# Optimization experiments

Hardware: AMD Instinct MI355X
Metric: run time of the kernel (lower is better)

The kernel has to match this reference:

```python
import jax, jax.numpy as jnp
import numpy as np

N, M, D = 65536, 1024, 2


def setup_inputs() -> dict:
    key = jax.random.key(0)
    k1, k2, k3 = jax.random.split(key, 3)
    sample = jax.random.uniform(k1, (N, D), dtype=jnp.float32)
    mu = jax.random.uniform(k2, (M, D), dtype=jnp.float32)
    # original init: A = 10 * I; add small noise so covariances are anisotropic
    A = 10.0 * jnp.broadcast_to(jnp.eye(D, dtype=jnp.float32), (M, D, D)) \
        + 0.1 * jax.random.normal(k3, (M, D, D), dtype=jnp.float32)
    w = jnp.ones((M, 1), dtype=jnp.float32)
    return {"sample": sample, "mu": mu, "A": A, "w": w}


def reference(sample, mu, A, w):
    # gamma_j = A_j @ A_j^T  -> precision matrices, (M, D, D)
    gamma = jnp.einsum('mde,mfe->mdf', A, A)
    # 2x2 determinant (only case implemented in the original module)
    det = gamma[:, 0, 0] * gamma[:, 1, 1] - gamma[:, 0, 1] * gamma[:, 1, 0]
    # log weights: log_softmax(w) + 0.5 * log det(gamma)
    log_w = jax.nn.log_softmax(w[:, 0], axis=0) + 0.5 * jnp.log(det)  # (M,)
    # Mahalanobis quadratic form q_ij = (x_i - mu_j)^T gamma_j (x_i - mu_j),
    # expanded to avoid materializing an (N, M, D) difference tensor.
    xGx = jnp.einsum('nd,mde,ne->nm', sample, gamma, sample)          # (N, M)
    gm = jnp.einsum('mde,me->md', gamma, mu)                          # (M, D)
    cross = sample @ gm.T                                             # (N, M)
    mGm = jnp.einsum('md,md->m', gm, mu)                              # (M,)
    q = xGx - 2.0 * cross + mGm[None, :]
    # log-likelihood per sample: logsumexp_j (log_w_j - q_ij)
    return jax.nn.logsumexp(log_w[None, :] - q, axis=1)               # (N,)
```

## Files before the change

### kernel.cpp

```cpp
#include <hip/hip_runtime.h>
#include <math.h>

#define LOG2E 1.4426950408889634f
#define LN2   0.6931471805599453f

static constexpr int M = 1024;
static constexpr int N = 65536;


__global__ __launch_bounds__(1024)
void gm_prep(const float* __restrict__ mu,
             const float* __restrict__ A,
             const float* __restrict__ w,
             float* __restrict__ ws) {
    __shared__ float red[1024];
    const int j = threadIdx.x;

    const float4 a = ((const float4*)A)[j];
    const float g00 = a.x*a.x + a.y*a.y;
    const float g01 = a.x*a.z + a.y*a.w;
    const float g11 = a.z*a.z + a.w*a.w;
    const float2 m  = ((const float2*)mu)[j];
    const float gm0 = g00*m.x + g01*m.y;
    const float gm1 = g01*m.x + g11*m.y;
    const float mGm = gm0*m.x + gm1*m.y;
    const float det = g00*g11 - g01*g01;
    const float wj  = w[j];

    red[j] = wj; __syncthreads();
    for (int off = 512; off > 0; off >>= 1) {
        if (j < off) red[j] = fmaxf(red[j], red[j+off]);
        __syncthreads();
    }
    const float wmax = red[0]; __syncthreads();
    red[j] = expf(wj - wmax); __syncthreads();
    for (int off = 512; off > 0; off >>= 1) {
        if (j < off) red[j] = red[j] + red[j+off];
        __syncthreads();
    }
    const float lse = wmax + logf(red[0]); __syncthreads();

    const float log_w = wj - lse + 0.5f * logf(det);

    red[j] = log_w; __syncthreads();
    for (int off = 512; off > 0; off >>= 1) {
        if (j < off) red[j] = fmaxf(red[j], red[j+off]);
        __syncthreads();
    }
    const float L = red[0];

    float* c = ws + j*8;
    c[0] = LOG2E * (log_w - mGm - L);
    c[1] = LOG2E * 2.0f * gm0;
    c[2] = LOG2E * 2.0f * gm1;
    c[3] = -LOG2E * g00;
    c[4] = -LOG2E * 2.0f * g01;
    c[5] = -LOG2E * g11;
    c[6] = 0.0f;
    c[7] = 0.0f;
    if (j == 0) ws[M*8] = LOG2E * L;
}

__global__ __launch_bounds__(256)
void gm_main(const float* __restrict__ sample,
             const float* __restrict__ ws,
             float* __restrict__ out) {
    __shared__ __align__(16) float coef[M*8];
    __shared__ float partial[256];
    __shared__ float sL2;
    const int t = threadIdx.x;

    const float4* wsv = (const float4*)ws;
    float4* cv = (float4*)coef;
    #pragma unroll
    for (int k = 0; k < 8; k++)
        cv[t + 256*k] = wsv[t + 256*k];
    if (t == 0) sL2 = ws[M*8];
    __syncthreads();

    const int lane  = t & 63;
    const int chunk = t >> 6;
    const int i = blockIdx.x*64 + lane;

    const float2 xy = ((const float2*)sample)[i];
    const float x0 = xy.x, x1 = xy.y;
    const float xx = x0*x0, xyp = x0*x1, yy = x1*x1;

    float s0 = 0.0f, s1 = 0.0f;
    const float* c = coef + chunk*256*8;
    #pragma unroll 8
    for (int jj = 0; jj < 256; jj++) {
        const float* cc = c + jj*8;
        const float v = fmaf(cc[5], yy,
                        fmaf(cc[4], xyp,
                        fmaf(cc[3], xx,
                        fmaf(cc[2], x1,
                        fmaf(cc[1], x0, cc[0])))));
        const float e = __builtin_amdgcn_exp2f(v);
        if (jj & 1) s1 += e; else s0 += e;
    }
    partial[t] = s0 + s1;
    __syncthreads();

    if (t < 64) {
        const float s = partial[t] + partial[t+64] + partial[t+128] + partial[t+192];
        out[blockIdx.x*64 + t] = LN2 * (sL2 + __builtin_amdgcn_logf(s));
    }
}

__global__ __launch_bounds__(256)
void gm_fused(const float* __restrict__ sample,
              const float* __restrict__ mu,
              const float* __restrict__ A,
              const float* __restrict__ w,
              float* __restrict__ out) {
    __shared__ __align__(16) float coef[M*8];
    __shared__ float red[256];
    const int t = threadIdx.x;

    float wv[4], c0t[4], c1t[4], c2t[4], c3t[4], c4t[4], c5t[4], dets[4];
    float wmaxl = -3.4e38f;
    #pragma unroll
    for (int k = 0; k < 4; k++) {
        wv[k] = w[t + 256*k];
        wmaxl = fmaxf(wmaxl, wv[k]);
    }
    red[t] = wmaxl; __syncthreads();
    for (int off = 128; off > 0; off >>= 1) {
        if (t < off) red[t] = fmaxf(red[t], red[t+off]);
        __syncthreads();
    }
    const float wmax = red[0]; __syncthreads();
    float se = 0.0f;
    #pragma unroll
    for (int k = 0; k < 4; k++) se += expf(wv[k] - wmax);
    red[t] = se; __syncthreads();
    for (int off = 128; off > 0; off >>= 1) {
        if (t < off) red[t] = red[t] + red[t+off];
        __syncthreads();
    }
    const float lse = wmax + logf(red[0]); __syncthreads();

    float Lml = -3.4e38f;
    float lwk[4];
    #pragma unroll
    for (int k = 0; k < 4; k++) {
        const int j = t + 256*k;
        const float4 a = ((const float4*)A)[j];
        const float g00 = a.x*a.x + a.y*a.y;
        const float g01 = a.x*a.z + a.y*a.w;
        const float g11 = a.z*a.z + a.w*a.w;
        const float2 m  = ((const float2*)mu)[j];
        const float gm0 = g00*m.x + g01*m.y;
        const float gm1 = g01*m.x + g11*m.y;
        const float mGm = gm0*m.x + gm1*m.y;
        dets[k] = g00*g11 - g01*g01;
        lwk[k]  = wv[k] - lse + 0.5f*logf(dets[k]);
        Lml = fmaxf(Lml, lwk[k]);
        c0t[k] = lwk[k] - mGm;
        c1t[k] = 2.0f*gm0;
        c2t[k] = 2.0f*gm1;
        c3t[k] = -g00;
        c4t[k] = -2.0f*g01;
        c5t[k] = -g11;
    }
    red[t] = Lml; __syncthreads();
    for (int off = 128; off > 0; off >>= 1) {
        if (t < off) red[t] = fmaxf(red[t], red[t+off]);
        __syncthreads();
    }
    const float L = red[0];
    #pragma unroll
    for (int k = 0; k < 4; k++) {
        float* c = coef + (t + 256*k)*8;
        c[0] = LOG2E*(c0t[k] - L);
        c[1] = LOG2E*c1t[k];
        c[2] = LOG2E*c2t[k];
        c[3] = LOG2E*c3t[k];
        c[4] = LOG2E*c4t[k];
        c[5] = LOG2E*c5t[k];
    }
    __syncthreads();

    const int i = blockIdx.x*256 + t;
    const float2 xy = ((const float2*)sample)[i];
    const float x0 = xy.x, x1 = xy.y;
    const float xx = x0*x0, xyp = x0*x1, yy = x1*x1;
    float s0 = 0.0f, s1 = 0.0f;
    #pragma unroll 8
    for (int jj = 0; jj < M; jj++) {
        const float* cc = coef + jj*8;
        const float v = fmaf(cc[5], yy,
                        fmaf(cc[4], xyp,
                        fmaf(cc[3], xx,
                        fmaf(cc[2], x1,
                        fmaf(cc[1], x0, cc[0])))));
        const float e = __builtin_amdgcn_exp2f(v);
        if (jj & 1) s1 += e; else s0 += e;
    }
    out[i] = LN2 * (LOG2E*L + __builtin_amdgcn_logf(s0 + s1));
}

extern "C" void kernel_launch(void* const* d_in, const int* in_sizes, int n_in,
                              void* d_out, int out_size, void* d_ws, size_t ws_size,
                              hipStream_t stream) {
    const float* sample = (const float*)d_in[0];
    const float* mu     = (const float*)d_in[1];
    const float* A      = (const float*)d_in[2];
    const float* w      = (const float*)d_in[3];
    float* out = (float*)d_out;

    if (ws_size >= (size_t)(M*8 + 1) * sizeof(float)) {
        gm_prep<<<1, 1024, 0, stream>>>(mu, A, w, (float*)d_ws);
        gm_main<<<N/64, 256, 0, stream>>>(sample, (const float*)d_ws, out);
    } else {
        gm_fused<<<N/256, 256, 0, stream>>>(sample, mu, A, w, out);
    }
}
```

Before: 80.41 us.

## Register-block four samples per thread and use wave shuffles in prep reductions

The main kernel now launches 1024-thread blocks that each cover 256 samples. Every thread holds four samples in registers and reuses each coefficient load from shared memory across all four, and the 16 waves each take 64 components before a shared-memory cross-wave sum. The prep kernel replaces its tree reductions over shared memory, which needed many barriers, with 64-lane shuffle reductions plus a 16-entry combine. This targets LDS bandwidth and the coefficient-staging overhead per block, at the cost of fewer blocks (256) and higher register pressure.

New measurement: 76.32 us. 5.1% less time.

```diff
diff --git a/kernel.cpp b/kernel.cpp
--- a/kernel.cpp
+++ b/kernel.cpp
@@ -7,14 +7,27 @@
 static constexpr int M = 1024;
 static constexpr int N = 65536;
 
+
+__device__ inline float wave_max64(float v) {
+    #pragma unroll
+    for (int o = 32; o > 0; o >>= 1) v = fmaxf(v, __shfl_xor(v, o));
+    return v;
+}
+__device__ inline float wave_sum64(float v) {
+    #pragma unroll
+    for (int o = 32; o > 0; o >>= 1) v += __shfl_xor(v, o);
+    return v;
+}
 
 __global__ __launch_bounds__(1024)
 void gm_prep(const float* __restrict__ mu,
              const float* __restrict__ A,
              const float* __restrict__ w,
              float* __restrict__ ws) {
-    __shared__ float red[1024];
-    const int j = threadIdx.x;
+    __shared__ float r[16];
+    const int j    = threadIdx.x;
+    const int lane = j & 63;
+    const int wv   = j >> 6;
 
     const float4 a = ((const float4*)A)[j];
     const float g00 = a.x*a.x + a.y*a.y;
@@ -27,27 +40,31 @@
     const float det = g00*g11 - g01*g01;
     const float wj  = w[j];
 
-    red[j] = wj; __syncthreads();
-    for (int off = 512; off > 0; off >>= 1) {
-        if (j < off) red[j] = fmaxf(red[j], red[j+off]);
-        __syncthreads();
-    }
-    const float wmax = red[0]; __syncthreads();
-    red[j] = expf(wj - wmax); __syncthreads();
-    for (int off = 512; off > 0; off >>= 1) {
-        if (j < off) red[j] = red[j] + red[j+off];
-        __syncthreads();
-    }
-    const float lse = wmax + logf(red[0]); __syncthreads();
+    float t = wave_max64(wj);
+    if (lane == 0) r[wv] = t;
+    __syncthreads();
+    float wmax = r[0];
+    #pragma unroll
+    for (int i = 1; i < 16; i++) wmax = fmaxf(wmax, r[i]);
+    __syncthreads();
+
+    t = wave_sum64(expf(wj - wmax));
+    if (lane == 0) r[wv] = t;
+    __syncthreads();
+    float se = 0.0f;
+    #pragma unroll
+    for (int i = 0; i < 16; i++) se += r[i];
+    const float lse = wmax + logf(se);
+    __syncthreads();
 
     const float log_w = wj - lse + 0.5f * logf(det);
 
-    red[j] = log_w; __syncthreads();
-    for (int off = 512; off > 0; off >>= 1) {
-        if (j < off) red[j] = fmaxf(red[j], red[j+off]);
-        __syncthreads();
-    }
-    const float L = red[0];
+    t = wave_max64(log_w);
+    if (lane == 0) r[wv] = t;
+    __syncthreads();
+    float L = r[0];
+    #pragma unroll
+    for (int i = 1; i < 16; i++) L = fmaxf(L, r[i]);
 
     float* c = ws + j*8;
     c[0] = LOG2E * (log_w - mGm - L);
@@ -61,50 +78,60 @@
     if (j == 0) ws[M*8] = LOG2E * L;
 }
 
-__global__ __launch_bounds__(256)
+__global__ __launch_bounds__(1024)
 void gm_main(const float* __restrict__ sample,
              const float* __restrict__ ws,
              float* __restrict__ out) {
     __shared__ __align__(16) float coef[M*8];
-    __shared__ float partial[256];
-    __shared__ float sL2;
+    __shared__ float partial[16*256];
     const int t = threadIdx.x;
 
     const float4* wsv = (const float4*)ws;
     float4* cv = (float4*)coef;
-    #pragma unroll
-    for (int k = 0; k < 8; k++)
-        cv[t + 256*k] = wsv[t + 256*k];
-    if (t == 0) sL2 = ws[M*8];
-    __syncthreads();
-
-    const int lane  = t & 63;
-    const int chunk = t >> 6;
-    const int i = blockIdx.x*64 + lane;
-
-    const float2 xy = ((const float2*)sample)[i];
-    const float x0 = xy.x, x1 = xy.y;
-    const float xx = x0*x0, xyp = x0*x1, yy = x1*x1;
-
-    float s0 = 0.0f, s1 = 0.0f;
-    const float* c = coef + chunk*256*8;
-    #pragma unroll 8
-    for (int jj = 0; jj < 256; jj++) {
+    cv[t]        = wsv[t];
+    cv[t + 1024] = wsv[t + 1024];
+    __syncthreads();
+
+    const int lane = t & 63;
+    const int wave = t >> 6;
+    const int base = blockIdx.x * 256;
+
+    float x0[4], x1[4], xx[4], xy[4], yy[4], acc[4];
+    #pragma unroll
+    for (int k = 0; k < 4; k++) {
+        const float2 p = ((const float2*)sample)[base + 64*k + lane];
+        x0[k] = p.x; x1[k] = p.y;
+        xx[k] = p.x*p.x; xy[k] = p.x*p.y; yy[k] = p.y*p.y;
+        acc[k] = 0.0f;
+    }
+
+    const float* c = coef + wave*64*8;
+    #pragma unroll 4
+    for (int jj = 0; jj < 64; jj++) {
         const float* cc = c + jj*8;
-        const float v = fmaf(cc[5], yy,
-                        fmaf(cc[4], xyp,
-                        fmaf(cc[3], xx,
-                        fmaf(cc[2], x1,
-                        fmaf(cc[1], x0, cc[0])))));
-        const float e = __builtin_amdgcn_exp2f(v);
-        if (jj & 1) s1 += e; else s0 += e;
-    }
-    partial[t] = s0 + s1;
-    __syncthreads();
-
-    if (t < 64) {
-        const float s = partial[t] + partial[t+64] + partial[t+128] + partial[t+192];
-        out[blockIdx.x*64 + t] = LN2 * (sL2 + __builtin_amdgcn_logf(s));
+        const float c0 = cc[0], c1 = cc[1], c2 = cc[2];
+        const float c3 = cc[3], c4 = cc[4], c5 = cc[5];
+        #pragma unroll
+        for (int k = 0; k < 4; k++) {
+            const float v = fmaf(c5, yy[k],
+                            fmaf(c4, xy[k],
+                            fmaf(c3, xx[k],
+                            fmaf(c2, x1[k],
+                            fmaf(c1, x0[k], c0)))));
+            acc[k] += __builtin_amdgcn_exp2f(v);
+        }
+    }
+
+    #pragma unroll
+    for (int k = 0; k < 4; k++)
+        partial[wave*256 + 64*k + lane] = acc[k];
+    __syncthreads();
+
+    if (t < 256) {
+        float s = 0.0f;
+        #pragma unroll
+        for (int w2 = 0; w2 < 16; w2++) s += partial[w2*256 + t];
+        out[base + t] = LN2 * (ws[M*8] + __builtin_amdgcn_logf(s));
     }
 }
 
@@ -118,13 +145,10 @@
     __shared__ float red[256];
     const int t = threadIdx.x;
 
-    float wv[4], c0t[4], c1t[4], c2t[4], c3t[4], c4t[4], c5t[4], dets[4];
+    float wv[4], c0t[4], c1t[4], c2t[4], c3t[4], c4t[4], c5t[4];
     float wmaxl = -3.4e38f;
     #pragma unroll
-    for (int k = 0; k < 4; k++) {
-        wv[k] = w[t + 256*k];
-        wmaxl = fmaxf(wmaxl, wv[k]);
-    }
+    for (int k = 0; k < 4; k++) { wv[k] = w[t + 256*k]; wmaxl = fmaxf(wmaxl, wv[k]); }
     red[t] = wmaxl; __syncthreads();
     for (int off = 128; off > 0; off >>= 1) {
         if (t < off) red[t] = fmaxf(red[t], red[t+off]);
@@ -142,7 +166,6 @@
     const float lse = wmax + logf(red[0]); __syncthreads();
 
     float Lml = -3.4e38f;
-    float lwk[4];
     #pragma unroll
     for (int k = 0; k < 4; k++) {
         const int j = t + 256*k;
@@ -154,15 +177,11 @@
         const float gm0 = g00*m.x + g01*m.y;
         const float gm1 = g01*m.x + g11*m.y;
         const float mGm = gm0*m.x + gm1*m.y;
-        dets[k] = g00*g11 - g01*g01;
-        lwk[k]  = wv[k] - lse + 0.5f*logf(dets[k]);
-        Lml = fmaxf(Lml, lwk[k]);
-        c0t[k] = lwk[k] - mGm;
-        c1t[k] = 2.0f*gm0;
-        c2t[k] = 2.0f*gm1;
-        c3t[k] = -g00;
-        c4t[k] = -2.0f*g01;
-        c5t[k] = -g11;
+        const float det = g00*g11 - g01*g01;
+        const float lw  = wv[k] - lse + 0.5f*logf(det);
+        Lml = fmaxf(Lml, lw);
+        c0t[k] = lw - mGm; c1t[k] = 2.0f*gm0; c2t[k] = 2.0f*gm1;
+        c3t[k] = -g00; c4t[k] = -2.0f*g01; c5t[k] = -g11;
     }
     red[t] = Lml; __syncthreads();
     for (int off = 128; off > 0; off >>= 1) {
@@ -173,12 +192,8 @@
     #pragma unroll
     for (int k = 0; k < 4; k++) {
         float* c = coef + (t + 256*k)*8;
-        c[0] = LOG2E*(c0t[k] - L);
-        c[1] = LOG2E*c1t[k];
-        c[2] = LOG2E*c2t[k];
-        c[3] = LOG2E*c3t[k];
-        c[4] = LOG2E*c4t[k];
-        c[5] = LOG2E*c5t[k];
+        c[0] = LOG2E*(c0t[k] - L); c[1] = LOG2E*c1t[k]; c[2] = LOG2E*c2t[k];
+        c[3] = LOG2E*c3t[k]; c[4] = LOG2E*c4t[k]; c[5] = LOG2E*c5t[k];
     }
     __syncthreads();
 
@@ -212,7 +227,7 @@
 
     if (ws_size >= (size_t)(M*8 + 1) * sizeof(float)) {
         gm_prep<<<1, 1024, 0, stream>>>(mu, A, w, (float*)d_ws);
-        gm_main<<<N/64, 256, 0, stream>>>(sample, (const float*)d_ws, out);
+        gm_main<<<N/256, 1024, 0, stream>>>(sample, (const float*)d_ws, out);
     } else {
         gm_fused<<<N/256, 256, 0, stream>>>(sample, mu, A, w, out);
     }
```
